# Performance work log

Measured on AMD Instinct MI355X. Metric: run time of the kernel, lower is better.

## Reference

```python
import jax, jax.numpy as jnp
import numpy as np

B, L, D, F = 8, 1024, 256, 11
TEMP = D ** 0.5
LN_EPS = 1e-6


def setup_inputs() -> dict:
    key = jax.random.key(0)
    ks = jax.random.split(key, 14)
    mk = lambda k, s: jax.random.normal(k, s, dtype=jnp.float32)
    return {
        "q": mk(ks[0], (B, L, D)),
        "k": mk(ks[1], (B, L, D)),
        "v": mk(ks[2], (B, L, D)),
        "x": jax.random.uniform(ks[3], (B, L, F), dtype=jnp.float32),
        "inputs_lengths": jax.random.randint(ks[4], (B,), 512, L + 1),
        "w_qs": mk(ks[5], (D, D)) * 0.05,
        "w_ks": mk(ks[6], (D, D)) * 0.05,
        "w_vs": mk(ks[7], (D, D)) * 0.05,
        "w_qs2": mk(ks[8], (D, D)) * 0.05,
        "w_ks2": mk(ks[9], (D, D)) * 0.05,
        "w_fc": mk(ks[10], (D, D)) * 0.05,
        "feature_importance": mk(ks[11], (F,)) * 0.1,
        "ln_gamma": jnp.ones((D,), jnp.float32),
        "ln_beta": jnp.zeros((D,), jnp.float32),
    }


def reference(q, k, v, x, w_qs, w_ks, w_vs, w_qs2, w_ks2, w_fc,
              feature_importance, ln_gamma, ln_beta, inputs_lengths):
    lin = lambda a, w: jnp.einsum('bli,oi->blo', a, w)  # torch Linear: y = x W^T
    qp = lin(q, w_qs)
    kp = lin(k, w_ks)
    vp = lin(v, w_vs)
    q2 = lin(q, w_qs2)
    k2 = lin(k, w_ks2)

    # key-position validity mask [B, L]
    key_mask = jnp.arange(L)[None, :] < inputs_lengths[:, None]

    # FeatureSim: pairwise L1 feature distances weighted by feature_importance
    fd = jnp.abs(x[:, :, None, :] - x[:, None, :, :])           # [B,L,L,F]
    fa = jnp.einsum('bijf,f->bij', fd, feature_importance)      # [B,L,L]
    fa = jnp.where(key_mask[:, None, :], fa, -jnp.inf)          # pad_masking
    fa = jax.nn.softmax(fa, axis=-1)
    fa = jnp.nan_to_num(fa)                                     # nan -> 0 for fully-masked rows

    # dual-score attention with tanh activation (no row normalization)
    attn = jnp.einsum('bid,bjd->bij', qp / TEMP, kp)
    q2f = jnp.einsum('bij,bjd->bid', fa, q2)
    k2f = jnp.einsum('bij,bjd->bid', fa, k2)
    attn = attn + jnp.einsum('bid,bjd->bij', q2f / TEMP, k2f)
    zm = key_mask[:, None, :]
    attn = jnp.where(zm, attn, 0.0)                             # pad_zero_masking
    attn = jnp.tanh(attn)
    attn = jnp.where(zm, attn, 0.0)                             # pad_zero_masking (tanh(0)=0, kept for fidelity)

    out = jnp.einsum('bij,bjd->bid', attn, vp)
    out = lin(out, w_fc) + q                                    # dropout is identity at eval
    mu = jnp.mean(out, axis=-1, keepdims=True)
    var = jnp.var(out, axis=-1, keepdims=True)
    out = (out - mu) / jnp.sqrt(var + LN_EPS) * ln_gamma + ln_beta
    return (out, attn)
```

## Files before the change

kernel.cpp:

```cpp
#include <hip/hip_runtime.h>
#include <hip/hip_bf16.h>
#include <math.h>

typedef __hip_bfloat16 bf16;
typedef __bf16 bf16x8 __attribute__((ext_vector_type(8)));
typedef float  f32x4  __attribute__((ext_vector_type(4)));

#define NB 8
#define SL 1024
#define DD 256
#define NF 11
#define RPB 8

__device__ __forceinline__ bf16x8 ldfrag(const bf16* p) {
  return *reinterpret_cast<const bf16x8*>(p);
}
__device__ __forceinline__ bf16x8 ldfrag(const float* p) {
  const float4 a = *reinterpret_cast<const float4*>(p);
  const float4 b = *reinterpret_cast<const float4*>(p + 4);
  bf16x8 r;
  r[0] = (__bf16)a.x; r[1] = (__bf16)a.y; r[2] = (__bf16)a.z; r[3] = (__bf16)a.w;
  r[4] = (__bf16)b.x; r[5] = (__bf16)b.y; r[6] = (__bf16)b.z; r[7] = (__bf16)b.w;
  return r;
}
__device__ __forceinline__ unsigned short us(float f) {
  bf16 h = __float2bfloat16(f);
  return *reinterpret_cast<unsigned short*>(&h);
}

template<typename T>
__device__ __forceinline__ void stage_tile(const T* __restrict__ g, int ld,
                                           bf16* __restrict__ s, int tid) {
#pragma unroll
  for (int it = 0; it < 4; ++it) {
    const int cid = it * 256 + tid;
    const int row = cid >> 3, c16 = cid & 7;
    bf16x8 v = ldfrag(g + (size_t)row * ld + c16 * 8);
    *reinterpret_cast<bf16x8*>(s + row * 64 + ((c16 ^ (row & 7)) << 3)) = v;
  }
}

__device__ __forceinline__ void compute_tiles(const bf16* __restrict__ sA,
                                              const bf16* __restrict__ sB,
                                              int lane, int wave, f32x4 acc[4][4]) {
  const int n15 = lane & 15, quad = lane >> 4;
  const int wm = (wave >> 1) * 64, wn = (wave & 1) * 64;
#pragma unroll
  for (int kc = 0; kc < 2; ++kc) {
    const int c16 = kc * 4 + quad;
    bf16x8 aF[4], bF[4];
#pragma unroll
    for (int t = 0; t < 4; ++t) {
      const int ra = wm + t * 16 + n15;
      aF[t] = *reinterpret_cast<const bf16x8*>(sA + ra * 64 + ((c16 ^ (ra & 7)) << 3));
      const int rb = wn + t * 16 + n15;
      bF[t] = *reinterpret_cast<const bf16x8*>(sB + rb * 64 + ((c16 ^ (rb & 7)) << 3));
    }
#pragma unroll
    for (int ti = 0; ti < 4; ++ti)
#pragma unroll
      for (int tj = 0; tj < 4; ++tj)
        acc[ti][tj] = __builtin_amdgcn_mfma_f32_16x16x32_bf16(aF[ti], bF[tj], acc[ti][tj], 0, 0, 0);
  }
}

template<typename TA, typename TB>
__device__ __forceinline__ void gemm_core(const TA* __restrict__ A, int lda,
                                          const TB* __restrict__ B, int ldb, int K,
                                          bf16* sA, bf16* sB, int tid, f32x4 acc[4][4]) {
  const int lane = tid & 63, wave = tid >> 6;
  for (int k0 = 0; k0 < K; k0 += 64) {
    stage_tile(A + k0, lda, sA, tid);
    stage_tile(B + k0, ldb, sB, tid);
    __syncthreads();
    compute_tiles(sA, sB, lane, wave, acc);
    __syncthreads();
  }
}

__device__ __forceinline__ float wred_sum(float v) {
#pragma unroll
  for (int o = 32; o > 0; o >>= 1) v += __shfl_xor(v, o, 64);
  return v;
}

__global__ __launch_bounds__(256) void k_proj(
    const float* __restrict__ q, const float* __restrict__ k, const float* __restrict__ v,
    const float* __restrict__ wqs, const float* __restrict__ wks, const float* __restrict__ wvs,
    const float* __restrict__ wqs2, const float* __restrict__ wks2,
    bf16* __restrict__ qp, bf16* __restrict__ kp,
    bf16* __restrict__ vpt, bf16* __restrict__ q2t, bf16* __restrict__ k2t)
{
  __shared__ bf16 sA[128 * 64], sB[128 * 64];
  const int tid = threadIdx.x, lane = tid & 63, wave = tid >> 6;
  const int z = blockIdx.z;
  const float* A = (z == 2) ? v : ((z == 1 || z == 4) ? k : q);
  const float* W = (z == 0) ? wqs : (z == 1) ? wks : (z == 2) ? wvs : (z == 3) ? wqs2 : wks2;
  const int rowBase = blockIdx.x * 128;
  const int colBase = blockIdx.y * 128;
  f32x4 acc[4][4] = {};
  gemm_core(A + (size_t)rowBase * DD, DD, W + (size_t)colBase * DD, DD, DD, sA, sB, tid, acc);
  const int n15 = lane & 15, quad = lane >> 4;
  const int wm = (wave >> 1) * 64, wn = (wave & 1) * 64;
  if (z <= 1) {
    bf16* O = (z == 0) ? qp : kp;
#pragma unroll
    for (int ti = 0; ti < 4; ++ti)
#pragma unroll
      for (int tj = 0; tj < 4; ++tj)
#pragma unroll
        for (int r = 0; r < 4; ++r) {
          int row = rowBase + wm + ti * 16 + quad * 4 + r;
          int col = colBase + wn + tj * 16 + n15;
          O[(size_t)row * DD + col] = __float2bfloat16(acc[ti][tj][r]);
        }
  } else {
    bf16* O = (z == 2) ? vpt : (z == 3) ? q2t : k2t;
    const int bb = rowBase >> 10, rowInB = rowBase & 1023;
#pragma unroll
    for (int ti = 0; ti < 4; ++ti)
#pragma unroll
      for (int tj = 0; tj < 4; ++tj) {
        int l0  = rowInB + wm + ti * 16 + quad * 4;
        int col = colBase + wn + tj * 16 + n15;
        ushort4 pk = make_ushort4(us(acc[ti][tj][0]), us(acc[ti][tj][1]),
                                  us(acc[ti][tj][2]), us(acc[ti][tj][3]));
        *reinterpret_cast<ushort4*>(&O[((size_t)bb * DD + col) * SL + l0]) = pk;
      }
  }
}

__global__ __launch_bounds__(256) void k_fa(const float* __restrict__ x,
                                            const float* __restrict__ fi_g,
                                            const int* __restrict__ lens,
                                            bf16* __restrict__ fa)
{
  __shared__ __align__(16) float sx[SL * NF];
  __shared__ float sredS[4][RPB];
  const int tid = threadIdx.x, wave = tid >> 6;
  const int b  = blockIdx.x >> 7;
  const int i0 = (blockIdx.x & 127) * RPB;
  {
    const float4* src = reinterpret_cast<const float4*>(x + (size_t)b * SL * NF);
    float4* dst = reinterpret_cast<float4*>(sx);
#pragma unroll
    for (int it = 0; it < 11; ++it) dst[it * 256 + tid] = src[it * 256 + tid];
  }
  float fiv[NF];
#pragma unroll
  for (int f = 0; f < NF; ++f) fiv[f] = fi_g[f];
  const int len = lens[b];
  __syncthreads();
  float xi[RPB][NF];
#pragma unroll
  for (int i = 0; i < RPB; ++i)
#pragma unroll
    for (int f = 0; f < NF; ++f) xi[i][f] = sx[(i0 + i) * NF + f];
  float e[RPB][4];
  float ps[RPB];
#pragma unroll
  for (int i = 0; i < RPB; ++i) ps[i] = 0.f;
#pragma unroll
  for (int t = 0; t < 4; ++t) {
    const int j = tid + t * 256;
    const bool valid = (t < 2) || (j < len);
    float xj[NF];
#pragma unroll
    for (int f = 0; f < NF; ++f) xj[f] = sx[j * NF + f];
#pragma unroll
    for (int i = 0; i < RPB; ++i) {
      float a = 0.f;
#pragma unroll
      for (int f = 0; f < NF; ++f) a += fabsf(xi[i][f] - xj[f]) * fiv[f];
      float ev = valid ? __expf(a) : 0.f;
      e[i][t] = ev;
      ps[i] += ev;
    }
  }
#pragma unroll
  for (int i = 0; i < RPB; ++i) {
    float wsv = wred_sum(ps[i]);
    if ((tid & 63) == 0) sredS[wave][i] = wsv;
  }
  __syncthreads();
  bf16* out = fa + (size_t)b * SL * SL + (size_t)i0 * SL;
#pragma unroll
  for (int i = 0; i < RPB; ++i) {
    const float inv = 1.f / (sredS[0][i] + sredS[1][i] + sredS[2][i] + sredS[3][i]);
#pragma unroll
    for (int t = 0; t < 4; ++t)
      out[(size_t)i * SL + tid + t * 256] = __float2bfloat16(e[i][t] * inv);
  }
}

__global__ __launch_bounds__(256) void k_famul(const bf16* __restrict__ fa,
                                               const bf16* __restrict__ q2t,
                                               const bf16* __restrict__ k2t,
                                               bf16* __restrict__ q2f,
                                               bf16* __restrict__ k2f)
{
  __shared__ bf16 sA[128 * 64], sB[128 * 64];
  const int tid = threadIdx.x, lane = tid & 63, wave = tid >> 6;
  const int b = blockIdx.z >> 1, which = blockIdx.z & 1;
  const int iBase = blockIdx.x * 128, dBase = blockIdx.y * 128;
  const bf16* A  = fa + (size_t)b * SL * SL + (size_t)iBase * SL;
  const bf16* Bm = (which ? k2t : q2t) + (size_t)b * DD * SL + (size_t)dBase * SL;
  f32x4 acc[4][4] = {};
  gemm_core(A, SL, Bm, SL, SL, sA, sB, tid, acc);
  bf16* O = (which ? k2f : q2f) + (size_t)b * SL * DD;
  const int n15 = lane & 15, quad = lane >> 4;
  const int wm = (wave >> 1) * 64, wn = (wave & 1) * 64;
#pragma unroll
  for (int ti = 0; ti < 4; ++ti)
#pragma unroll
    for (int tj = 0; tj < 4; ++tj)
#pragma unroll
      for (int r = 0; r < 4; ++r)
        O[(size_t)(iBase + wm + ti * 16 + quad * 4 + r) * DD +
          dBase + wn + tj * 16 + n15] = __float2bfloat16(acc[ti][tj][r]);
}

__global__ __launch_bounds__(256) void k_attn(const bf16* __restrict__ qp,
                                              const bf16* __restrict__ kp,
                                              const bf16* __restrict__ q2f,
                                              const bf16* __restrict__ k2f,
                                              const int* __restrict__ lens,
                                              float* __restrict__ attn_f32)
{
  __shared__ bf16 sA[128 * 64], sB[128 * 64];
  const int tid = threadIdx.x, lane = tid & 63, wave = tid >> 6;
  const int b = blockIdx.z;
  const int iBase = blockIdx.x * 128, jBase = blockIdx.y * 128;
  f32x4 acc[4][4] = {};
  gemm_core(qp  + ((size_t)b * SL + iBase) * DD, DD,
            kp  + ((size_t)b * SL + jBase) * DD, DD, DD, sA, sB, tid, acc);
  gemm_core(q2f + ((size_t)b * SL + iBase) * DD, DD,
            k2f + ((size_t)b * SL + jBase) * DD, DD, DD, sA, sB, tid, acc);
  const int len = lens[b];
  const int n15 = lane & 15, quad = lane >> 4;
  const int wm = (wave >> 1) * 64, wn = (wave & 1) * 64;
#pragma unroll
  for (int ti = 0; ti < 4; ++ti)
#pragma unroll
    for (int tj = 0; tj < 4; ++tj)
#pragma unroll
      for (int r = 0; r < 4; ++r) {
        int i = iBase + wm + ti * 16 + quad * 4 + r;
        int j = jBase + wn + tj * 16 + n15;
        float vv = (j < len) ? tanhf(acc[ti][tj][r] * (1.f / 16.f)) : 0.f;
        attn_f32[(size_t)b * SL * SL + (size_t)i * SL + j] = vv;
      }
}

__global__ __launch_bounds__(256) void k_av(const float* __restrict__ attn,
                                            const bf16* __restrict__ vpt,
                                            bf16* __restrict__ out_pre)
{
  __shared__ bf16 sA[128 * 64], sB[128 * 64];
  const int tid = threadIdx.x, lane = tid & 63, wave = tid >> 6;
  const int b = blockIdx.z;
  const int iBase = blockIdx.x * 128, dBase = blockIdx.y * 128;
  f32x4 acc[4][4] = {};
  gemm_core(attn + (size_t)b * SL * SL + (size_t)iBase * SL, SL,
            vpt  + (size_t)b * DD * SL + (size_t)dBase * SL, SL, SL, sA, sB, tid, acc);
  bf16* O = out_pre + (size_t)b * SL * DD;
  const int n15 = lane & 15, quad = lane >> 4;
  const int wm = (wave >> 1) * 64, wn = (wave & 1) * 64;
#pragma unroll
  for (int ti = 0; ti < 4; ++ti)
#pragma unroll
    for (int tj = 0; tj < 4; ++tj)
#pragma unroll
      for (int r = 0; r < 4; ++r)
        O[(size_t)(iBase + wm + ti * 16 + quad * 4 + r) * DD +
          dBase + wn + tj * 16 + n15] = __float2bfloat16(acc[ti][tj][r]);
}

__global__ __launch_bounds__(256) void k_fc(const bf16* __restrict__ out_pre,
                                            const float* __restrict__ wfc,
                                            const float* __restrict__ qres,
                                            float* __restrict__ fcout)
{
  __shared__ bf16 sA[128 * 64], sB[128 * 64];
  const int tid = threadIdx.x, lane = tid & 63, wave = tid >> 6;
  const int rowBase = blockIdx.x * 128, colBase = blockIdx.y * 128;
  f32x4 acc[4][4] = {};
  gemm_core(out_pre + (size_t)rowBase * DD, DD, wfc + (size_t)colBase * DD, DD, DD,
            sA, sB, tid, acc);
  const int n15 = lane & 15, quad = lane >> 4;
  const int wm = (wave >> 1) * 64, wn = (wave & 1) * 64;
#pragma unroll
  for (int ti = 0; ti < 4; ++ti)
#pragma unroll
    for (int tj = 0; tj < 4; ++tj)
#pragma unroll
      for (int r = 0; r < 4; ++r) {
        int row = rowBase + wm + ti * 16 + quad * 4 + r;
        int col = colBase + wn + tj * 16 + n15;
        fcout[(size_t)row * DD + col] = acc[ti][tj][r] + qres[(size_t)row * DD + col];
      }
}

__global__ __launch_bounds__(256) void k_ln(const float* __restrict__ fcout,
                                            const float* __restrict__ gam,
                                            const float* __restrict__ bet,
                                            float* __restrict__ outp)
{
  __shared__ float r1[4], r2[4];
  const int r = blockIdx.x, tid = threadIdx.x;
  const float v = fcout[(size_t)r * DD + tid];
  float s = wred_sum(v), ss = wred_sum(v * v);
  if ((tid & 63) == 0) { r1[tid >> 6] = s; r2[tid >> 6] = ss; }
  __syncthreads();
  s  = r1[0] + r1[1] + r1[2] + r1[3];
  ss = r2[0] + r2[1] + r2[2] + r2[3];
  const float mean = s * (1.f / DD);
  const float var  = ss * (1.f / DD) - mean * mean;
  float y = (v - mean) * rsqrtf(var + 1e-6f);
  y = y * gam[tid] + bet[tid];
  outp[(size_t)r * DD + tid] = y;
}

extern "C" void kernel_launch(void* const* d_in, const int* in_sizes, int n_in,
                              void* d_out, int out_size, void* d_ws, size_t ws_size,
                              hipStream_t stream)
{
  const float* q    = (const float*)d_in[0];
  const float* k    = (const float*)d_in[1];
  const float* v    = (const float*)d_in[2];
  const float* x    = (const float*)d_in[3];
  const int*  lens  = (const int*)d_in[4];
  const float* wqs  = (const float*)d_in[5];
  const float* wks  = (const float*)d_in[6];
  const float* wvs  = (const float*)d_in[7];
  const float* wqs2 = (const float*)d_in[8];
  const float* wks2 = (const float*)d_in[9];
  const float* wfc  = (const float*)d_in[10];
  const float* fi   = (const float*)d_in[11];
  const float* gam  = (const float*)d_in[12];
  const float* bet  = (const float*)d_in[13];

  char* w = (char*)d_ws;
  const size_t MB = 1u << 20;
  bf16* qp   = (bf16*)(w + 0 * MB);
  bf16* kp   = (bf16*)(w + 4 * MB);
  bf16* vpt  = (bf16*)(w + 8 * MB);
  bf16* q2t  = (bf16*)(w + 12 * MB);
  bf16* k2t  = (bf16*)(w + 16 * MB);
  bf16* q2f  = (bf16*)(w + 20 * MB);
  bf16* k2f  = (bf16*)(w + 24 * MB);
  bf16* fa   = (bf16*)(w + 28 * MB);
  bf16* out_pre = q2t;
  float* fcout  = (float*)(w + 0 * MB);

  float* outp  = (float*)d_out;
  float* attnp = outp + (size_t)NB * SL * DD;

  dim3 blk(256);
  hipLaunchKernelGGL(k_proj,  dim3(64, 2, 5),  blk, 0, stream,
                     q, k, v, wqs, wks, wvs, wqs2, wks2, qp, kp, vpt, q2t, k2t);
  hipLaunchKernelGGL(k_fa,    dim3(NB * 128),  blk, 0, stream, x, fi, lens, fa);
  hipLaunchKernelGGL(k_famul, dim3(8, 2, 16),  blk, 0, stream, fa, q2t, k2t, q2f, k2f);
  hipLaunchKernelGGL(k_attn,  dim3(8, 8, 8),   blk, 0, stream,
                     qp, kp, q2f, k2f, lens, attnp);
  hipLaunchKernelGGL(k_av,    dim3(8, 2, 8),   blk, 0, stream, attnp, vpt, out_pre);
  hipLaunchKernelGGL(k_fc,    dim3(64, 2),     blk, 0, stream, out_pre, wfc, q, fcout);
  hipLaunchKernelGGL(k_ln,    dim3(NB * SL),   blk, 0, stream, fcout, gam, bet, outp);
}
```

Measured before the change: 217.6 us.

## Use direct global-to-LDS loads for bf16 tiles and bf16 attention copy for AV

The bf16 tile staging now uses the global_load_lds builtin so data goes straight from global memory into LDS, with the XOR swizzle applied on the source address instead of the LDS address. The attention kernel also writes a bf16 copy of the attention matrix into the reused fa buffer. The AV GEMM reads that copy instead of the fp32 output, which halves its read traffic and routes it through the direct-to-LDS path. The cost is an extra 16 MB of bf16 writes in k_attn, and correctness depends on the per-wave contiguous layout of the LDS destination.

```diff
diff --git a/kernel.cpp b/kernel.cpp
--- a/kernel.cpp
+++ b/kernel.cpp
@@ -11,6 +11,9 @@
 #define DD 256
 #define NF 11
 #define RPB 8
+
+#define AS_G __attribute__((address_space(1)))
+#define AS_L __attribute__((address_space(3)))
 
 __device__ __forceinline__ bf16x8 ldfrag(const bf16* p) {
   return *reinterpret_cast<const bf16x8*>(p);
@@ -28,15 +31,28 @@
   return *reinterpret_cast<unsigned short*>(&h);
 }
 
-template<typename T>
-__device__ __forceinline__ void stage_tile(const T* __restrict__ g, int ld,
-                                           bf16* __restrict__ s, int tid) {
+__device__ __forceinline__ void stage_any(const float* __restrict__ g, int ld,
+                                          bf16* __restrict__ s, int tid) {
 #pragma unroll
   for (int it = 0; it < 4; ++it) {
     const int cid = it * 256 + tid;
     const int row = cid >> 3, c16 = cid & 7;
     bf16x8 v = ldfrag(g + (size_t)row * ld + c16 * 8);
     *reinterpret_cast<bf16x8*>(s + row * 64 + ((c16 ^ (row & 7)) << 3)) = v;
+  }
+}
+
+__device__ __forceinline__ void stage_any(const bf16* __restrict__ g, int ld,
+                                          bf16* __restrict__ s, int tid) {
+  const int wbase = tid & ~63;
+#pragma unroll
+  for (int it = 0; it < 4; ++it) {
+    const int cid = it * 256 + tid;
+    const int row = cid >> 3, sc = cid & 7;
+    const int c16 = sc ^ (row & 7);
+    const bf16* src = g + (size_t)row * ld + c16 * 8;
+    bf16* dst = s + (size_t)(it * 256 + wbase) * 8;
+    __builtin_amdgcn_global_load_lds((const AS_G void*)src, (AS_L void*)dst, 16, 0, 0);
   }
 }
 
@@ -70,8 +86,8 @@
                                           bf16* sA, bf16* sB, int tid, f32x4 acc[4][4]) {
   const int lane = tid & 63, wave = tid >> 6;
   for (int k0 = 0; k0 < K; k0 += 64) {
-    stage_tile(A + k0, lda, sA, tid);
-    stage_tile(B + k0, ldb, sB, tid);
+    stage_any(A + k0, lda, sA, tid);
+    stage_any(B + k0, ldb, sB, tid);
     __syncthreads();
     compute_tiles(sA, sB, lane, wave, acc);
     __syncthreads();
@@ -225,7 +241,8 @@
                                               const bf16* __restrict__ q2f,
                                               const bf16* __restrict__ k2f,
                                               const int* __restrict__ lens,
-                                              float* __restrict__ attn_f32)
+                                              float* __restrict__ attn_f32,
+                                              bf16* __restrict__ attn_b16)
 {
   __shared__ bf16 sA[128 * 64], sB[128 * 64];
   const int tid = threadIdx.x, lane = tid & 63, wave = tid >> 6;
@@ -248,11 +265,13 @@
         int i = iBase + wm + ti * 16 + quad * 4 + r;
         int j = jBase + wn + tj * 16 + n15;
         float vv = (j < len) ? tanhf(acc[ti][tj][r] * (1.f / 16.f)) : 0.f;
-        attn_f32[(size_t)b * SL * SL + (size_t)i * SL + j] = vv;
+        size_t idx = (size_t)b * SL * SL + (size_t)i * SL + j;
+        attn_f32[idx] = vv;
+        attn_b16[idx] = __float2bfloat16(vv);
       }
 }
 
-__global__ __launch_bounds__(256) void k_av(const float* __restrict__ attn,
+__global__ __launch_bounds__(256) void k_av(const bf16* __restrict__ attn,
                                             const bf16* __restrict__ vpt,
                                             bf16* __restrict__ out_pre)
 {
@@ -350,6 +369,7 @@
   bf16* q2f  = (bf16*)(w + 20 * MB);
   bf16* k2f  = (bf16*)(w + 24 * MB);
   bf16* fa   = (bf16*)(w + 28 * MB);
+  bf16* attn_b16 = fa;
   bf16* out_pre = q2t;
   float* fcout  = (float*)(w + 0 * MB);
 
@@ -362,8 +382,8 @@
   hipLaunchKernelGGL(k_fa,    dim3(NB * 128),  blk, 0, stream, x, fi, lens, fa);
   hipLaunchKernelGGL(k_famul, dim3(8, 2, 16),  blk, 0, stream, fa, q2t, k2t, q2f, k2f);
   hipLaunchKernelGGL(k_attn,  dim3(8, 8, 8),   blk, 0, stream,
-                     qp, kp, q2f, k2f, lens, attnp);
-  hipLaunchKernelGGL(k_av,    dim3(8, 2, 8),   blk, 0, stream, attnp, vpt, out_pre);
+                     qp, kp, q2f, k2f, lens, attnp, attn_b16);
+  hipLaunchKernelGGL(k_av,    dim3(8, 2, 8),   blk, 0, stream, attn_b16, vpt, out_pre);
   hipLaunchKernelGGL(k_fc,    dim3(64, 2),     blk, 0, stream, out_pre, wfc, q, fcout);
   hipLaunchKernelGGL(k_ln,    dim3(NB * SL),   blk, 0, stream, fcout, gam, bet, outp);
 }
```

Result: no change. 217.9 us (+0.1%).
